# Kernel tuning notes

Hardware: AMD Instinct MI355X
Metric: run time of the kernel (lower is better)

## Reference

```python
import jax, jax.numpy as jnp
import numpy as np

N_QUBITS = 8
N_LAYERS = 4


def setup_inputs() -> dict:
    key = jax.random.key(0)
    k_x, k_rot, k_ent, k_w, k_b = jax.random.split(key, 5)
    B, S, F = 64, 8192, 64
    x = jax.random.normal(k_x, (B, S, F), dtype=jnp.float32)
    rotation_params = jax.random.normal(k_rot, (N_LAYERS, N_QUBITS, 3), dtype=jnp.float32) * 0.01
    entangle_params = jax.random.normal(k_ent, (N_LAYERS, N_QUBITS - 1), dtype=jnp.float32) * 0.01
    proj_w = jax.random.normal(k_w, (N_QUBITS * 2, N_QUBITS), dtype=jnp.float32) * (1.0 / np.sqrt(N_QUBITS))
    proj_b = jax.random.normal(k_b, (N_QUBITS * 2,), dtype=jnp.float32) * 0.01
    return {"x": x, "rotation_params": rotation_params, "entangle_params": entangle_params,
            "proj_w": proj_w, "proj_b": proj_b}


def reference(x, rotation_params, entangle_params, proj_w, proj_b):
    n_layers, n_qubits, _ = rotation_params.shape
    # amplitude encoding: tanh of first n_qubits features -> [B, S, Q]
    qs = jnp.tanh(x[..., :n_qubits])
    for layer in range(n_layers):
        r = rotation_params[layer]  # [Q, 3]
        # rx, ry, rz are each (cos+sin)*state -> fused per-qubit scale
        scale = ((jnp.cos(r[:, 0]) + jnp.sin(r[:, 0]))
                 * (jnp.cos(r[:, 1]) + jnp.sin(r[:, 1]))
                 * (jnp.cos(r[:, 2]) + jnp.sin(r[:, 2])))  # [Q]
        rz = qs * scale  # broadcast over [B, S, Q]
        # entanglement: entangled[..., i] = rz[i]*(1-w_i) + rz[i+1]*w_i, last qubit unchanged
        w = jax.nn.sigmoid(entangle_params[layer])  # [Q-1]
        front = rz[..., :-1] * (1.0 - w) + rz[..., 1:] * w
        qs = jnp.concatenate([front, rz[..., -1:]], axis=-1)
    # projection Linear(Q -> 2Q)
    return jnp.einsum('bsq,oq->bso', qs, proj_w) + proj_b
```

## Files before the change

kernel.cpp:

```cpp
#include <hip/hip_runtime.h>

#define NQ 8
#define NL 4
#define NO 16

typedef __attribute__((ext_vector_type(4))) float float4v;

__global__ __launch_bounds__(256) void qcl_fused(
    const float* __restrict__ x,
    const float* __restrict__ rot,
    const float* __restrict__ ent,
    const float* __restrict__ pw,
    const float* __restrict__ pb,
    float* __restrict__ out,
    int n_rows)
{
    __shared__ float sW[NO][NQ];
    __shared__ float sB[NO];
    const int tid = threadIdx.x;

    if (tid < NO) {
        float W[NQ];
        #pragma unroll
        for (int q = 0; q < NQ; ++q) W[q] = pw[tid * NQ + q];

        #pragma unroll
        for (int l = NL - 1; l >= 0; --l) {
            float wl[NQ - 1];
            #pragma unroll
            for (int i = 0; i < NQ - 1; ++i) {
                float e = __expf(-ent[l * (NQ - 1) + i]);
                wl[i] = __builtin_amdgcn_rcpf(1.0f + e);
            }
            float WE[NQ];
            WE[0] = W[0] * (1.0f - wl[0]);
            #pragma unroll
            for (int j = 1; j < NQ - 1; ++j)
                WE[j] = W[j] * (1.0f - wl[j]) + W[j - 1] * wl[j - 1];
            WE[NQ - 1] = W[NQ - 1] + W[NQ - 2] * wl[NQ - 2];
            #pragma unroll
            for (int q = 0; q < NQ; ++q) {
                float r0 = rot[(l * NQ + q) * 3 + 0];
                float r1 = rot[(l * NQ + q) * 3 + 1];
                float r2 = rot[(l * NQ + q) * 3 + 2];
                float s = (__cosf(r0) + __sinf(r0)) *
                          (__cosf(r1) + __sinf(r1)) *
                          (__cosf(r2) + __sinf(r2));
                W[q] = WE[q] * s;
            }
        }
        #pragma unroll
        for (int q = 0; q < NQ; ++q) sW[tid][q] = W[q];
        sB[tid] = pb[tid];
    }
    __syncthreads();

    const int r = blockIdx.x * 256 + tid;
    if (r >= n_rows) return;

    const float4v* xp = (const float4v*)(x + (size_t)r * 64);
    float4v x0 = xp[0];
    float4v x1 = xp[1];
    float xs[NQ] = {x0.x, x0.y, x0.z, x0.w, x1.x, x1.y, x1.z, x1.w};

    float t[NQ];
    #pragma unroll
    for (int q = 0; q < NQ; ++q) {
        float e = __expf(2.0f * xs[q]);
        t[q] = 1.0f - 2.0f * __builtin_amdgcn_rcpf(e + 1.0f);
    }

    float acc[NO];
    #pragma unroll
    for (int o = 0; o < NO; ++o) {
        float a = sB[o];
        #pragma unroll
        for (int q = 0; q < NQ; ++q) a += sW[o][q] * t[q];
        acc[o] = a;
    }

    float4v* ov = (float4v*)(out + (size_t)r * NO);
    #pragma unroll
    for (int i = 0; i < 4; ++i) {
        float4v v;
        v.x = acc[4 * i + 0];
        v.y = acc[4 * i + 1];
        v.z = acc[4 * i + 2];
        v.w = acc[4 * i + 3];
        ov[i] = v;
    }
}

extern "C" void kernel_launch(void* const* d_in, const int* in_sizes, int n_in,
                              void* d_out, int out_size, void* d_ws, size_t ws_size,
                              hipStream_t stream) {
    const float* x   = (const float*)d_in[0];
    const float* rot = (const float*)d_in[1];
    const float* ent = (const float*)d_in[2];
    const float* pw  = (const float*)d_in[3];
    const float* pb  = (const float*)d_in[4];
    float* out = (float*)d_out;

    const int n_rows = in_sizes[0] / 64;
    const int block = 256;
    const int grid = (n_rows + block - 1) / block;
    hipLaunchKernelGGL(qcl_fused, dim3(grid), dim3(block), 0, stream,
                       x, rot, ent, pw, pb, out, n_rows);
}
```

Measured before the change: 28.89 us.

## Split each row across two lanes with shuffle exchange and two rows per thread

Each row's 8 input features and 16 outputs are now split between a pair of adjacent lanes. Each lane loads one float4 and computes the tanh for its half, then swaps the halves with a lane shuffle. Each lane produces 8 of the 16 outputs, so a wavefront's loads and stores cover denser contiguous chunks, which should improve coalescing of the strided 256-byte row accesses. Each thread also handles two half-rows a grid-stride apart, which halves the grid and adds memory-level parallelism. The cost is the shuffle and select instructions plus some duplicated setup work.

Result: faster. 27.35 us (-5.4%).

```diff
diff --git a/kernel.cpp b/kernel.cpp
--- a/kernel.cpp
+++ b/kernel.cpp
@@ -55,39 +55,68 @@
     }
     __syncthreads();
 
-    const int r = blockIdx.x * 256 + tid;
-    if (r >= n_rows) return;
+    const int nhalf = n_rows * 2;
+    const int H = gridDim.x * 256;
+    const int gid = blockIdx.x * 256 + tid;
+    const int h = tid & 1;
 
-    const float4v* xp = (const float4v*)(x + (size_t)r * 64);
-    float4v x0 = xp[0];
-    float4v x1 = xp[1];
-    float xs[NQ] = {x0.x, x0.y, x0.z, x0.w, x1.x, x1.y, x1.z, x1.w};
+    const int g0 = gid;
+    const int g1 = gid + H;
+    const bool v0 = g0 < nhalf;
+    const bool v1 = g1 < nhalf;
 
-    float t[NQ];
+    float4v a0 = {0.f, 0.f, 0.f, 0.f};
+    float4v a1 = {0.f, 0.f, 0.f, 0.f};
+    if (v0) a0 = *(const float4v*)(x + (size_t)(g0 >> 1) * 64 + h * 4);
+    if (v1) a1 = *(const float4v*)(x + (size_t)(g1 >> 1) * 64 + h * 4);
+
+    float m0[4], m1[4];
     #pragma unroll
-    for (int q = 0; q < NQ; ++q) {
-        float e = __expf(2.0f * xs[q]);
-        t[q] = 1.0f - 2.0f * __builtin_amdgcn_rcpf(e + 1.0f);
+    for (int j = 0; j < 4; ++j) {
+        float e0 = __expf(2.0f * a0[j]);
+        m0[j] = 1.0f - 2.0f * __builtin_amdgcn_rcpf(e0 + 1.0f);
+        float e1 = __expf(2.0f * a1[j]);
+        m1[j] = 1.0f - 2.0f * __builtin_amdgcn_rcpf(e1 + 1.0f);
     }
 
-    float acc[NO];
+    float tA[8], tB[8];
     #pragma unroll
-    for (int o = 0; o < NO; ++o) {
-        float a = sB[o];
-        #pragma unroll
-        for (int q = 0; q < NQ; ++q) a += sW[o][q] * t[q];
-        acc[o] = a;
+    for (int j = 0; j < 4; ++j) {
+        float o0 = __shfl_xor(m0[j], 1, 64);
+        float o1 = __shfl_xor(m1[j], 1, 64);
+        tA[j]     = h ? o0 : m0[j];
+        tA[j + 4] = h ? m0[j] : o0;
+        tB[j]     = h ? o1 : m1[j];
+        tB[j + 4] = h ? m1[j] : o1;
     }
 
-    float4v* ov = (float4v*)(out + (size_t)r * NO);
+    const int base = h * 8;
+    float accA[8], accB[8];
     #pragma unroll
-    for (int i = 0; i < 4; ++i) {
-        float4v v;
-        v.x = acc[4 * i + 0];
-        v.y = acc[4 * i + 1];
-        v.z = acc[4 * i + 2];
-        v.w = acc[4 * i + 3];
-        ov[i] = v;
+    for (int j = 0; j < 8; ++j) {
+        float aA = sB[base + j];
+        float aB = aA;
+        #pragma unroll
+        for (int q = 0; q < NQ; ++q) {
+            float w = sW[base + j][q];
+            aA += w * tA[q];
+            aB += w * tB[q];
+        }
+        accA[j] = aA;
+        accB[j] = aB;
+    }
+
+    if (v0) {
+        float4v* p = (float4v*)(out + (size_t)(g0 >> 1) * 16 + base);
+        float4v u0 = {accA[0], accA[1], accA[2], accA[3]};
+        float4v u1 = {accA[4], accA[5], accA[6], accA[7]};
+        p[0] = u0; p[1] = u1;
+    }
+    if (v1) {
+        float4v* p = (float4v*)(out + (size_t)(g1 >> 1) * 16 + base);
+        float4v u0 = {accB[0], accB[1], accB[2], accB[3]};
+        float4v u1 = {accB[4], accB[5], accB[6], accB[7]};
+        p[0] = u0; p[1] = u1;
     }
 }
 
@@ -102,8 +131,9 @@
     float* out = (float*)d_out;
 
     const int n_rows = in_sizes[0] / 64;
+    const int nhalf = n_rows * 2;
     const int block = 256;
-    const int grid = (n_rows + block - 1) / block;
+    const int grid = (nhalf + block * 2 - 1) / (block * 2);
     hipLaunchKernelGGL(qcl_fused, dim3(grid), dim3(block), 0, stream,
                        x, rot, ent, pw, pb, out, n_rows);
 }
```
